# Kernel tuning notes

Hardware: AMD Instinct MI355X
Metric: run time of the kernel (lower is better)

The kernel has to match this reference:

```python
import jax, jax.numpy as jnp
import numpy as np

B, C, H, W = 4, 64, 256, 256
ALPHA = 1.0


def _directional_scan(x, w, b, axis, reverse):
    """IRNN recurrence along `axis` of x [B,C,H,W].
    Boundary element = raw input; then h_t = relu(w_c*h_{t-1} + b_c + x_t).
    w, b: per-channel scalars [C]. reverse=True scans from the far edge.
    """
    xs = jnp.moveaxis(x, axis, 0)  # [L, B, C, K]
    if reverse:
        xs = xs[::-1]
    wb = w[None, :, None]  # broadcast over [B, C, K]
    bb = b[None, :, None]

    def step(h, xt):
        h = jax.nn.relu(wb * h + bb + xt)
        return h, h

    h0 = xs[0]  # boundary: raw input, matching CUDA irnn init output=input.clone()
    _, ys = jax.lax.scan(step, h0, xs[1:])
    ys = jnp.concatenate([h0[None], ys], axis=0)
    if reverse:
        ys = ys[::-1]
    return jnp.moveaxis(ys, 0, axis)


def setup_inputs() -> dict:
    key = jax.random.key(0)
    ks = jax.random.split(key, 5)
    inp = {
        "input": jax.random.normal(ks[0], (B, C, H, W), dtype=jnp.float32),
        # depthwise 1x1 conv weights are one scalar per channel, init = alpha
        "w_up": jnp.full((C,), ALPHA, dtype=jnp.float32),
        "w_right": jnp.full((C,), ALPHA, dtype=jnp.float32),
        "w_down": jnp.full((C,), ALPHA, dtype=jnp.float32),
        "w_left": jnp.full((C,), ALPHA, dtype=jnp.float32),
        "b_up": jax.random.normal(ks[1], (C,), dtype=jnp.float32) * 0.01,
        "b_right": jax.random.normal(ks[2], (C,), dtype=jnp.float32) * 0.01,
        "b_down": jax.random.normal(ks[3], (C,), dtype=jnp.float32) * 0.01,
        "b_left": jax.random.normal(ks[4], (C,), dtype=jnp.float32) * 0.01,
    }
    return inp


def reference(input, w_up, w_right, w_down, w_left, b_up, b_right, b_down, b_left):
    # up: information flows bottom->top (scan rows from bottom)
    up = _directional_scan(input, w_up, b_up, axis=2, reverse=True)
    # right: flows left->right (scan cols forward)
    right = _directional_scan(input, w_right, b_right, axis=3, reverse=False)
    # down: flows top->bottom (scan rows forward)
    down = _directional_scan(input, w_down, b_down, axis=2, reverse=False)
    # left: flows right->left (scan cols from right)
    left = _directional_scan(input, w_left, b_left, axis=3, reverse=True)
    return jnp.stack([up, right, down, left], axis=0)  # [4,B,C,H,W]
```

## Files before the change

### kernel.cpp

```cpp
#include <hip/hip_runtime.h>

#define NB 4
#define NC 64
#define NH 256
#define NW 256
#define PLANE ((long)NB * NC * NH * NW)

__global__ __launch_bounds__(256) void irnn_fused(
    const float* __restrict__ x,
    const float* __restrict__ w_up,    const float* __restrict__ b_up,
    const float* __restrict__ w_right, const float* __restrict__ b_right,
    const float* __restrict__ w_down,  const float* __restrict__ b_down,
    const float* __restrict__ w_left,  const float* __restrict__ b_left,
    float* __restrict__ out)
{
    __shared__ float tile[256 * 33];

    const int dir = blockIdx.y;
    const int t   = threadIdx.x;

    if (dir == 0 || dir == 2) {
        int tid = blockIdx.x * 256 + t;
        int w   = tid & (NW - 1);
        int bc  = tid >> 8;
        int c   = bc & (NC - 1);
        long base = (long)bc * (NH * NW) + w;
        float* o = out + (long)dir * PLANE;

        if (dir == 2) {
            float wc = w_down[c], bb = b_down[c];
            float h = x[base];
            o[base] = h;
            long idx = base;
            for (int batch = 0; batch < 31; ++batch) {
                float v[8];
                #pragma unroll
                for (int k = 0; k < 8; ++k) v[k] = x[idx + (long)(k + 1) * NW];
                #pragma unroll
                for (int k = 0; k < 8; ++k) {
                    h = fmaxf(wc * h + bb + v[k], 0.0f);
                    o[idx + (long)(k + 1) * NW] = h;
                }
                idx += 8L * NW;
            }
            float v[7];
            #pragma unroll
            for (int k = 0; k < 7; ++k) v[k] = x[idx + (long)(k + 1) * NW];
            #pragma unroll
            for (int k = 0; k < 7; ++k) {
                h = fmaxf(wc * h + bb + v[k], 0.0f);
                o[idx + (long)(k + 1) * NW] = h;
            }
        } else {
            float wc = w_up[c], bb = b_up[c];
            long idx = base + (long)(NH - 1) * NW;
            float h = x[idx];
            o[idx] = h;
            for (int batch = 0; batch < 31; ++batch) {
                float v[8];
                #pragma unroll
                for (int k = 0; k < 8; ++k) v[k] = x[idx - (long)(k + 1) * NW];
                #pragma unroll
                for (int k = 0; k < 8; ++k) {
                    h = fmaxf(wc * h + bb + v[k], 0.0f);
                    o[idx - (long)(k + 1) * NW] = h;
                }
                idx -= 8L * NW;
            }
            float v[7];
            #pragma unroll
            for (int k = 0; k < 7; ++k) v[k] = x[idx - (long)(k + 1) * NW];
            #pragma unroll
            for (int k = 0; k < 7; ++k) {
                h = fmaxf(wc * h + bb + v[k], 0.0f);
                o[idx - (long)(k + 1) * NW] = h;
            }
        }
    } else {
        const int bc = blockIdx.x;
        const int c  = bc & (NC - 1);
        const bool fwd = (dir == 1);
        const float wc = fwd ? w_right[c] : w_left[c];
        const float bb = fwd ? b_right[c] : b_left[c];
        float* o = out + (long)dir * PLANE;
        const long slab = (long)bc * (NH * NW);

        const int r  = t >> 3;
        const int c4 = t & 7;

        float h = 0.0f;
        for (int ci = 0; ci < 8; ++ci) {
            const int w0 = fwd ? ci * 32 : 224 - ci * 32;

            #pragma unroll
            for (int k = 0; k < 8; ++k) {
                int row = r + 32 * k;
                float4 v = *(const float4*)(x + slab + (long)row * NW + w0 + c4 * 4);
                float* dst = &tile[row * 33 + c4 * 4];
                dst[0] = v.x; dst[1] = v.y; dst[2] = v.z; dst[3] = v.w;
            }
            __syncthreads();

            float* myrow = &tile[t * 33];
            if (fwd) {
                int v0 = 0;
                if (ci == 0) { h = myrow[0]; v0 = 1; }
                for (int v = v0; v < 32; ++v) {
                    float xv = myrow[v];
                    h = fmaxf(wc * h + bb + xv, 0.0f);
                    myrow[v] = h;
                }
            } else {
                int v0 = 31;
                if (ci == 0) { h = myrow[31]; v0 = 30; }
                for (int v = v0; v >= 0; --v) {
                    float xv = myrow[v];
                    h = fmaxf(wc * h + bb + xv, 0.0f);
                    myrow[v] = h;
                }
            }
            __syncthreads();

            #pragma unroll
            for (int k = 0; k < 8; ++k) {
                int row = r + 32 * k;
                const float* src = &tile[row * 33 + c4 * 4];
                float4 v;
                v.x = src[0]; v.y = src[1]; v.z = src[2]; v.w = src[3];
                *(float4*)(o + slab + (long)row * NW + w0 + c4 * 4) = v;
            }
            __syncthreads();
        }
    }
}

extern "C" void kernel_launch(void* const* d_in, const int* in_sizes, int n_in,
                              void* d_out, int out_size, void* d_ws, size_t ws_size,
                              hipStream_t stream) {
    const float* x       = (const float*)d_in[0];
    const float* w_up    = (const float*)d_in[1];
    const float* w_right = (const float*)d_in[2];
    const float* w_down  = (const float*)d_in[3];
    const float* w_left  = (const float*)d_in[4];
    const float* b_up    = (const float*)d_in[5];
    const float* b_right = (const float*)d_in[6];
    const float* b_down  = (const float*)d_in[7];
    const float* b_left  = (const float*)d_in[8];
    float* out = (float*)d_out;

    dim3 grid(256, 4);
    irnn_fused<<<grid, 256, 0, stream>>>(
        x, w_up, b_up, w_right, b_right, w_down, b_down, w_left, b_left, out);
}
```

Before: 346.2 us.

## Replace horizontal scans with wavefront parallel max-affine prefix scan, fuse left/right

Horizontal (left/right) scans are now computed with a warp-level parallel prefix scan. Each step is written as a composable max-affine map, with one wavefront per row and four columns per lane, so each thread no longer walks 32-column chunks serially through shared memory. Left and right are fused so each input row is read once and both outputs are written, and the vertical scans now use float2 per thread with half as many blocks. This removes the serial per-row dependency chain and the shared-memory barriers, at the cost of extra shuffle and arithmetic work. The composed maps may also round slightly differently from the sequential recurrence.

```diff
diff --git a/kernel.cpp b/kernel.cpp
--- a/kernel.cpp
+++ b/kernel.cpp
@@ -5,6 +5,7 @@
 #define NH 256
 #define NW 256
 #define PLANE ((long)NB * NC * NH * NW)
+#define HW    ((long)NH * NW)
 
 __global__ __launch_bounds__(256) void irnn_fused(
     const float* __restrict__ x,
@@ -14,122 +15,145 @@
     const float* __restrict__ w_left,  const float* __restrict__ b_left,
     float* __restrict__ out)
 {
-    __shared__ float tile[256 * 33];
+    const int t   = threadIdx.x;
+    const int blk = blockIdx.x;
 
-    const int dir = blockIdx.y;
-    const int t   = threadIdx.x;
+    if (blk < 256) {
+        const bool up  = blk < 128;
+        const int  tid = (blk & 127) * 256 + t;
+        const int  w2  = (tid & 127) << 1;
+        const int  bc  = tid >> 7;
+        const int  c   = bc & (NC - 1);
+        const long base = (long)bc * HW + w2;
+        const float wc = up ? w_up[c] : w_down[c];
+        const float bb = up ? b_up[c] : b_down[c];
+        float* o = out + (up ? 0L : 2L) * PLANE;
+        const long stp = up ? -(long)NW : (long)NW;
+        long idx = up ? base + (long)(NH - 1) * NW : base;
 
-    if (dir == 0 || dir == 2) {
-        int tid = blockIdx.x * 256 + t;
-        int w   = tid & (NW - 1);
-        int bc  = tid >> 8;
-        int c   = bc & (NC - 1);
-        long base = (long)bc * (NH * NW) + w;
-        float* o = out + (long)dir * PLANE;
-
-        if (dir == 2) {
-            float wc = w_down[c], bb = b_down[c];
-            float h = x[base];
-            o[base] = h;
-            long idx = base;
-            for (int batch = 0; batch < 31; ++batch) {
-                float v[8];
-                #pragma unroll
-                for (int k = 0; k < 8; ++k) v[k] = x[idx + (long)(k + 1) * NW];
-                #pragma unroll
-                for (int k = 0; k < 8; ++k) {
-                    h = fmaxf(wc * h + bb + v[k], 0.0f);
-                    o[idx + (long)(k + 1) * NW] = h;
-                }
-                idx += 8L * NW;
+        float2 h = *(const float2*)(x + idx);
+        *(float2*)(o + idx) = h;
+        for (int batch = 0; batch < 31; ++batch) {
+            float2 v[8];
+            #pragma unroll
+            for (int k = 0; k < 8; ++k)
+                v[k] = *(const float2*)(x + idx + (long)(k + 1) * stp);
+            #pragma unroll
+            for (int k = 0; k < 8; ++k) {
+                h.x = fmaxf(wc * h.x + bb + v[k].x, 0.0f);
+                h.y = fmaxf(wc * h.y + bb + v[k].y, 0.0f);
+                *(float2*)(o + idx + (long)(k + 1) * stp) = h;
             }
-            float v[7];
-            #pragma unroll
-            for (int k = 0; k < 7; ++k) v[k] = x[idx + (long)(k + 1) * NW];
-            #pragma unroll
-            for (int k = 0; k < 7; ++k) {
-                h = fmaxf(wc * h + bb + v[k], 0.0f);
-                o[idx + (long)(k + 1) * NW] = h;
-            }
-        } else {
-            float wc = w_up[c], bb = b_up[c];
-            long idx = base + (long)(NH - 1) * NW;
-            float h = x[idx];
-            o[idx] = h;
-            for (int batch = 0; batch < 31; ++batch) {
-                float v[8];
-                #pragma unroll
-                for (int k = 0; k < 8; ++k) v[k] = x[idx - (long)(k + 1) * NW];
-                #pragma unroll
-                for (int k = 0; k < 8; ++k) {
-                    h = fmaxf(wc * h + bb + v[k], 0.0f);
-                    o[idx - (long)(k + 1) * NW] = h;
-                }
-                idx -= 8L * NW;
-            }
-            float v[7];
-            #pragma unroll
-            for (int k = 0; k < 7; ++k) v[k] = x[idx - (long)(k + 1) * NW];
-            #pragma unroll
-            for (int k = 0; k < 7; ++k) {
-                h = fmaxf(wc * h + bb + v[k], 0.0f);
-                o[idx - (long)(k + 1) * NW] = h;
-            }
+            idx += 8L * stp;
+        }
+        float2 v[7];
+        #pragma unroll
+        for (int k = 0; k < 7; ++k)
+            v[k] = *(const float2*)(x + idx + (long)(k + 1) * stp);
+        #pragma unroll
+        for (int k = 0; k < 7; ++k) {
+            h.x = fmaxf(wc * h.x + bb + v[k].x, 0.0f);
+            h.y = fmaxf(wc * h.y + bb + v[k].y, 0.0f);
+            *(float2*)(o + idx + (long)(k + 1) * stp) = h;
         }
     } else {
-        const int bc = blockIdx.x;
-        const int c  = bc & (NC - 1);
-        const bool fwd = (dir == 1);
-        const float wc = fwd ? w_right[c] : w_left[c];
-        const float bb = fwd ? b_right[c] : b_left[c];
-        float* o = out + (long)dir * PLANE;
-        const long slab = (long)bc * (NH * NW);
+        const int lane = t & 63;
+        const int wv   = (blk - 256) * 4 + (t >> 6);
+        const int bc   = wv >> 6;
+        const int c    = bc & (NC - 1);
+        const int h0   = (wv & 63) * 4;
+        const float wr = w_right[c], br = b_right[c];
+        const float wl = w_left[c],  bl = b_left[c];
+        float* oR = out + 1L * PLANE;
+        float* oL = out + 3L * PLANE;
 
-        const int r  = t >> 3;
-        const int c4 = t & 7;
+        long rowb = (long)bc * HW + (long)h0 * NW;
+        float4 v = *(const float4*)(x + rowb + lane * 4);
 
-        float h = 0.0f;
-        for (int ci = 0; ci < 8; ++ci) {
-            const int w0 = fwd ? ci * 32 : 224 - ci * 32;
+        #pragma unroll
+        for (int rr = 0; rr < 4; ++rr) {
+            float4 vn = v;
+            if (rr < 3) vn = *(const float4*)(x + rowb + NW + lane * 4);
 
+            float cc, mm, dd;
+            float4 r;
+
+            if (lane == 0) {
+                float h = v.x;                      r.x = h;
+                h = fmaxf(wr * h + br + v.y, 0.0f); r.y = h;
+                h = fmaxf(wr * h + br + v.z, 0.0f); r.z = h;
+                h = fmaxf(wr * h + br + v.w, 0.0f); r.w = h;
+                cc = h; mm = 0.0f; dd = h;
+            } else {
+                cc = 0.0f; mm = wr; dd = br + v.x;
+                float a;
+                a = br + v.y; cc = fmaxf(0.0f, wr * cc + a); dd = wr * dd + a; mm *= wr;
+                a = br + v.z; cc = fmaxf(0.0f, wr * cc + a); dd = wr * dd + a; mm *= wr;
+                a = br + v.w; cc = fmaxf(0.0f, wr * cc + a); dd = wr * dd + a; mm *= wr;
+            }
             #pragma unroll
-            for (int k = 0; k < 8; ++k) {
-                int row = r + 32 * k;
-                float4 v = *(const float4*)(x + slab + (long)row * NW + w0 + c4 * 4);
-                float* dst = &tile[row * 33 + c4 * 4];
-                dst[0] = v.x; dst[1] = v.y; dst[2] = v.z; dst[3] = v.w;
-            }
-            __syncthreads();
-
-            float* myrow = &tile[t * 33];
-            if (fwd) {
-                int v0 = 0;
-                if (ci == 0) { h = myrow[0]; v0 = 1; }
-                for (int v = v0; v < 32; ++v) {
-                    float xv = myrow[v];
-                    h = fmaxf(wc * h + bb + xv, 0.0f);
-                    myrow[v] = h;
-                }
-            } else {
-                int v0 = 31;
-                if (ci == 0) { h = myrow[31]; v0 = 30; }
-                for (int v = v0; v >= 0; --v) {
-                    float xv = myrow[v];
-                    h = fmaxf(wc * h + bb + xv, 0.0f);
-                    myrow[v] = h;
+            for (int off = 1; off < 64; off <<= 1) {
+                float pc = __shfl_up(cc, off, 64);
+                float pm = __shfl_up(mm, off, 64);
+                float pd = __shfl_up(dd, off, 64);
+                if (lane >= off) {
+                    cc = fmaxf(cc, mm * pc + dd);
+                    dd = mm * pd + dd;
+                    mm = mm * pm;
                 }
             }
-            __syncthreads();
+            {
+                float pc = __shfl_up(cc, 1, 64);
+                float pd = __shfl_up(dd, 1, 64);
+                if (lane > 0) {
+                    float h = fmaxf(pc, pd);
+                    h = fmaxf(wr * h + br + v.x, 0.0f); r.x = h;
+                    h = fmaxf(wr * h + br + v.y, 0.0f); r.y = h;
+                    h = fmaxf(wr * h + br + v.z, 0.0f); r.z = h;
+                    h = fmaxf(wr * h + br + v.w, 0.0f); r.w = h;
+                }
+            }
+            *(float4*)(oR + rowb + lane * 4) = r;
 
+            if (lane == 63) {
+                float h = v.w;                      r.w = h;
+                h = fmaxf(wl * h + bl + v.z, 0.0f); r.z = h;
+                h = fmaxf(wl * h + bl + v.y, 0.0f); r.y = h;
+                h = fmaxf(wl * h + bl + v.x, 0.0f); r.x = h;
+                cc = h; mm = 0.0f; dd = h;
+            } else {
+                cc = 0.0f; mm = wl; dd = bl + v.w;
+                float a;
+                a = bl + v.z; cc = fmaxf(0.0f, wl * cc + a); dd = wl * dd + a; mm *= wl;
+                a = bl + v.y; cc = fmaxf(0.0f, wl * cc + a); dd = wl * dd + a; mm *= wl;
+                a = bl + v.x; cc = fmaxf(0.0f, wl * cc + a); dd = wl * dd + a; mm *= wl;
+            }
             #pragma unroll
-            for (int k = 0; k < 8; ++k) {
-                int row = r + 32 * k;
-                const float* src = &tile[row * 33 + c4 * 4];
-                float4 v;
-                v.x = src[0]; v.y = src[1]; v.z = src[2]; v.w = src[3];
-                *(float4*)(o + slab + (long)row * NW + w0 + c4 * 4) = v;
+            for (int off = 1; off < 64; off <<= 1) {
+                float pc = __shfl_down(cc, off, 64);
+                float pm = __shfl_down(mm, off, 64);
+                float pd = __shfl_down(dd, off, 64);
+                if (lane + off < 64) {
+                    cc = fmaxf(cc, mm * pc + dd);
+                    dd = mm * pd + dd;
+                    mm = mm * pm;
+                }
             }
-            __syncthreads();
+            {
+                float pc = __shfl_down(cc, 1, 64);
+                float pd = __shfl_down(dd, 1, 64);
+                if (lane < 63) {
+                    float h = fmaxf(pc, pd);
+                    h = fmaxf(wl * h + bl + v.w, 0.0f); r.w = h;
+                    h = fmaxf(wl * h + bl + v.z, 0.0f); r.z = h;
+                    h = fmaxf(wl * h + bl + v.y, 0.0f); r.y = h;
+                    h = fmaxf(wl * h + bl + v.x, 0.0f); r.x = h;
+                }
+            }
+            *(float4*)(oL + rowb + lane * 4) = r;
+
+            rowb += NW;
+            v = vn;
         }
     }
 }
@@ -148,7 +172,7 @@
     const float* b_left  = (const float*)d_in[8];
     float* out = (float*)d_out;
 
-    dim3 grid(256, 4);
+    dim3 grid(256 + 4096);
     irnn_fused<<<grid, 256, 0, stream>>>(
         x, w_up, b_up, w_right, b_right, w_down, b_down, w_left, b_left, out);
 }
```

New measurement: 334.5 us. 3.4% less time.
